# Kernel tuning notes

Hardware: AMD Instinct MI355X
Metric: run time of the kernel (lower is better)

Reference implementation:

```python
import jax, jax.numpy as jnp
import numpy as np

B, T = 4, 2048
IN_H, OUT_H = 4096, 4096   # in_hidden_size = output features, out_hidden_size = input features (torch F.linear quirk)
RANK = 1024


def setup_inputs() -> dict:
    key = jax.random.key(0)
    kx, ku, ks, kv, kb = jax.random.split(key, 5)
    x = jax.random.normal(kx, (B, T, OUT_H), dtype=jnp.float32)
    U = jax.random.normal(ku, (IN_H, RANK), dtype=jnp.float32) * 0.02
    S = jax.random.uniform(ks, (RANK,), dtype=jnp.float32)
    V = jax.random.normal(kv, (OUT_H, RANK), dtype=jnp.float32) * 0.02
    bias = jax.random.normal(kb, (IN_H,), dtype=jnp.float32) * 0.01
    return {"x": x, "U": U, "S": S, "V": V, "bias": bias}


def reference(x, U, S, V, bias):
    # Faithful to torch: M = U @ diag(S) @ V.T  (shape [in_hidden, out_hidden]);
    # F.linear(x, M, bias) = x @ M.T + bias, so x:[...,out_hidden] -> out:[...,in_hidden]
    M = (U * S) @ V.T                     # [IN_H, OUT_H]; (U*S) == U @ diag(S)
    return jnp.einsum('bto,io->bti', x, M) + bias
```

## Files before the change

### kernel.cpp

```cpp
#include <hip/hip_runtime.h>
#include <stdint.h>

typedef __attribute__((ext_vector_type(4))) float  floatx4;
typedef __attribute__((ext_vector_type(8))) short  short8;
typedef __attribute__((ext_vector_type(8))) __bf16 bf16x8;

__device__ __forceinline__ unsigned short f2bf(float f) {
  unsigned int u = __builtin_bit_cast(unsigned int, f);
  u += 0x7fffu + ((u >> 16) & 1u);
  return (unsigned short)(u >> 16);
}

typedef const __attribute__((address_space(1))) void* gptr_t;
typedef __attribute__((address_space(3))) void*       lptr_t;

__global__ __launch_bounds__(256) void prep_fused(
    const float* __restrict__ X, const float* __restrict__ V,
    const float* __restrict__ U, const float* __restrict__ S,
    unsigned short* __restrict__ Xb, unsigned short* __restrict__ Vt,
    unsigned short* __restrict__ Ub,
    int castBlocks, int transTotal, int transGX, int vrows, int vcols,
    unsigned int rankMask) {
  __shared__ float tile[32][33];
  int bid = blockIdx.x;
  int tid = threadIdx.x;
  if (bid < castBlocks) {
    size_t i = ((size_t)bid * 256 + tid) * 8;
    const floatx4* p = (const floatx4*)(X + i);
    floatx4 a = p[0], b = p[1];
    union { unsigned short us[8]; short8 v; } o;
    o.us[0] = f2bf(a[0]); o.us[1] = f2bf(a[1]); o.us[2] = f2bf(a[2]); o.us[3] = f2bf(a[3]);
    o.us[4] = f2bf(b[0]); o.us[5] = f2bf(b[1]); o.us[6] = f2bf(b[2]); o.us[7] = f2bf(b[3]);
    *(short8*)(Xb + i) = o.v;
  } else if (bid < castBlocks + transTotal) {
    int b  = bid - castBlocks;
    int bx = (b % transGX) * 32;
    int by = (b / transGX) * 32;
    int tx = tid & 31;
    int ty = tid >> 5;
    for (int i = ty; i < 32; i += 8)
      tile[i][tx] = V[(size_t)(by + i) * vcols + bx + tx];
    __syncthreads();
    for (int i = ty; i < 32; i += 8)
      Vt[(size_t)(bx + i) * vrows + by + tx] = f2bf(tile[tx][i]);
  } else {
    int b = bid - castBlocks - transTotal;
    size_t i = ((size_t)b * 256 + tid) * 4;
    floatx4 u = *(const floatx4*)(U + i);
    floatx4 s = *(const floatx4*)(S + (i & (size_t)rankMask));
    union { unsigned short us[4]; unsigned long long v; } o;
    o.us[0] = f2bf(u[0] * s[0]); o.us[1] = f2bf(u[1] * s[1]);
    o.us[2] = f2bf(u[2] * s[2]); o.us[3] = f2bf(u[3] * s[3]);
    *(unsigned long long*)(Ub + i) = o.v;
  }
}

__global__ __launch_bounds__(256, 2)
void gemm1_kernel(const unsigned short* __restrict__ A,
                  const unsigned short* __restrict__ Bt,
                  unsigned short* __restrict__ C,
                  int N, int K, int GX) {
  __shared__ unsigned short sA[2][128 * 32];
  __shared__ unsigned short sB[2][128 * 32];

  const int tid  = threadIdx.x;
  const int lane = tid & 63;
  const int wave = tid >> 6;
  const int wm = (wave >> 1) * 64;
  const int wn = (wave & 1) * 64;

  unsigned bid  = blockIdx.x;
  unsigned bw   = 8u * GX;
  unsigned band = bid / bw, rem = bid % bw;
  unsigned by   = band * 8 + (rem & 7u);
  unsigned bx   = rem >> 3;
  const int row0 = by * 128, col0 = bx * 128;

  floatx4 acc[4][4];
#pragma unroll
  for (int i = 0; i < 4; ++i)
#pragma unroll
    for (int j = 0; j < 4; ++j) acc[i][j] = (floatx4){0.f, 0.f, 0.f, 0.f};

  const unsigned short* Ablk = A + (size_t)row0 * K;
  const unsigned short* Bblk = Bt + (size_t)col0 * K;

  const int r0 = tid >> 2, c0 = (tid & 3) * 8;
  const int ldso0 = (wave * 64) * 8;
  const int ldso1 = (256 + wave * 64) * 8;
  const int mrow = lane & 15, quad = lane >> 4;

  for (int k0 = 0; k0 < K; k0 += 64) {
#pragma unroll
    for (int t = 0; t < 2; ++t) {
      const int kk = k0 + t * 32;
      __builtin_amdgcn_global_load_lds((gptr_t)(Ablk + (size_t)r0 * K + kk + c0),
                                       (lptr_t)(sA[t] + ldso0), 16, 0, 0);
      __builtin_amdgcn_global_load_lds((gptr_t)(Ablk + (size_t)(r0 + 64) * K + kk + c0),
                                       (lptr_t)(sA[t] + ldso1), 16, 0, 0);
      __builtin_amdgcn_global_load_lds((gptr_t)(Bblk + (size_t)r0 * K + kk + c0),
                                       (lptr_t)(sB[t] + ldso0), 16, 0, 0);
      __builtin_amdgcn_global_load_lds((gptr_t)(Bblk + (size_t)(r0 + 64) * K + kk + c0),
                                       (lptr_t)(sB[t] + ldso1), 16, 0, 0);
    }
    __syncthreads();
#pragma unroll
    for (int t = 0; t < 2; ++t) {
      bf16x8 af[4], bfr[4];
#pragma unroll
      for (int mi = 0; mi < 4; ++mi)
        af[mi] = __builtin_bit_cast(bf16x8,
                  *(const short8*)(sA[t] + (wm + mi * 16 + mrow) * 32 + quad * 8));
#pragma unroll
      for (int ni = 0; ni < 4; ++ni)
        bfr[ni] = __builtin_bit_cast(bf16x8,
                  *(const short8*)(sB[t] + (wn + ni * 16 + mrow) * 32 + quad * 8));
#pragma unroll
      for (int mi = 0; mi < 4; ++mi)
#pragma unroll
        for (int ni = 0; ni < 4; ++ni)
          acc[mi][ni] = __builtin_amdgcn_mfma_f32_16x16x32_bf16(af[mi], bfr[ni],
                                                                acc[mi][ni], 0, 0, 0);
    }
    __syncthreads();
  }

  const int orow = row0 + wm + quad * 4;
  const int ocol = col0 + wn + mrow;
#pragma unroll
  for (int mi = 0; mi < 4; ++mi)
#pragma unroll
    for (int r = 0; r < 4; ++r) {
      size_t rowoff = (size_t)(orow + mi * 16 + r) * N;
#pragma unroll
      for (int ni = 0; ni < 4; ++ni)
        C[rowoff + ocol + ni * 16] = f2bf(acc[mi][ni][r]);
    }
}

__global__ __launch_bounds__(256, 2)
void gemm2_kernel(const unsigned short* __restrict__ A,
                  const unsigned short* __restrict__ Bt,
                  float* __restrict__ C, const float* __restrict__ bias,
                  int N, int K, int GX) {
  __shared__ unsigned short sA[256 * 32];
  __shared__ unsigned short sB[128 * 32];

  const int tid  = threadIdx.x;
  const int lane = tid & 63;
  const int wave = tid >> 6;
  const int wm = (wave >> 1) * 128;
  const int wn = (wave & 1) * 64;

  unsigned bid  = blockIdx.x;
  unsigned bw   = 8u * GX;
  unsigned band = bid / bw, rem = bid % bw;
  unsigned by   = band * 8 + (rem & 7u);
  unsigned bx   = rem >> 3;
  const int row0 = by * 256, col0 = bx * 128;

  floatx4 acc[8][4];
#pragma unroll
  for (int i = 0; i < 8; ++i)
#pragma unroll
    for (int j = 0; j < 4; ++j) acc[i][j] = (floatx4){0.f, 0.f, 0.f, 0.f};

  const unsigned short* Ablk = A + (size_t)row0 * K;
  const unsigned short* Bblk = Bt + (size_t)col0 * K;

  const int r0 = tid >> 2, c0 = (tid & 3) * 8;
  const int mrow = lane & 15, quad = lane >> 4;

  for (int k0 = 0; k0 < K; k0 += 32) {
#pragma unroll
    for (int j = 0; j < 4; ++j)
      __builtin_amdgcn_global_load_lds((gptr_t)(Ablk + (size_t)(r0 + j * 64) * K + k0 + c0),
                                       (lptr_t)(sA + (j * 256 + wave * 64) * 8), 16, 0, 0);
#pragma unroll
    for (int j = 0; j < 2; ++j)
      __builtin_amdgcn_global_load_lds((gptr_t)(Bblk + (size_t)(r0 + j * 64) * K + k0 + c0),
                                       (lptr_t)(sB + (j * 256 + wave * 64) * 8), 16, 0, 0);
    __syncthreads();

    bf16x8 af[8], bfr[4];
#pragma unroll
    for (int mi = 0; mi < 8; ++mi)
      af[mi] = __builtin_bit_cast(bf16x8,
                *(const short8*)(sA + (wm + mi * 16 + mrow) * 32 + quad * 8));
#pragma unroll
    for (int ni = 0; ni < 4; ++ni)
      bfr[ni] = __builtin_bit_cast(bf16x8,
                *(const short8*)(sB + (wn + ni * 16 + mrow) * 32 + quad * 8));
#pragma unroll
    for (int mi = 0; mi < 8; ++mi)
#pragma unroll
      for (int ni = 0; ni < 4; ++ni)
        acc[mi][ni] = __builtin_amdgcn_mfma_f32_16x16x32_bf16(af[mi], bfr[ni],
                                                              acc[mi][ni], 0, 0, 0);
    __syncthreads();
  }

  const int orow = row0 + wm + quad * 4;
  const int ocol = col0 + wn + mrow;
  float bv[4];
#pragma unroll
  for (int ni = 0; ni < 4; ++ni) bv[ni] = bias[ocol + ni * 16];
#pragma unroll
  for (int mi = 0; mi < 8; ++mi)
#pragma unroll
    for (int r = 0; r < 4; ++r) {
      size_t rowoff = (size_t)(orow + mi * 16 + r) * N;
#pragma unroll
      for (int ni = 0; ni < 4; ++ni)
        C[rowoff + ocol + ni * 16] = acc[mi][ni][r] + bv[ni];
    }
}

extern "C" void kernel_launch(void* const* d_in, const int* in_sizes, int n_in,
                              void* d_out, int out_size, void* d_ws, size_t ws_size,
                              hipStream_t stream) {
  const float* x    = (const float*)d_in[0];
  const float* U    = (const float*)d_in[1];
  const float* S    = (const float*)d_in[2];
  const float* V    = (const float*)d_in[3];
  const float* bias = (const float*)d_in[4];

  const int RANK = in_sizes[2];
  const int INH  = in_sizes[4];
  const int OUTH = in_sizes[3] / RANK;
  const int M    = in_sizes[0] / OUTH;

  unsigned short* Xb = (unsigned short*)d_ws;
  unsigned short* Vt = Xb + (size_t)M * OUTH;
  unsigned short* Ub = Vt + (size_t)RANK * OUTH;
  unsigned short* Yb = Ub + (size_t)INH * RANK;

  const int castBlocks = (int)(((size_t)M * OUTH) / 2048);
  const int transGX    = RANK / 32;
  const int transTotal = transGX * (OUTH / 32);
  const int prepUBlk   = (int)(((size_t)INH * RANK) / 1024);
  prep_fused<<<castBlocks + transTotal + prepUBlk, 256, 0, stream>>>(
      x, V, U, S, Xb, Vt, Ub, castBlocks, transTotal, transGX, OUTH, RANK,
      (unsigned)(RANK - 1));

  gemm1_kernel<<<(M / 128) * (RANK / 128), 256, 0, stream>>>(
      Xb, Vt, Yb, RANK, OUTH, RANK / 128);

  gemm2_kernel<<<(M / 256) * (INH / 128), 256, 0, stream>>>(
      Yb, Ub, (float*)d_out, bias, INH, RANK, INH / 128);
}
```

Baseline: 407.0 us.

## Restructure gemm2 with 256x256 tiles, 512 threads, double-buffered K=64 swizzled LDS

The second GEMM moves from a 256x128 tile with 4 waves to a 256x256 tile with 8 waves. It also uses a BK=64, double-buffered LDS pipeline with an XOR swizzle, prefetches two stages ahead, and raises wave priority around the MFMA bursts. The aim is to hide global-to-LDS load latency behind compute, cut LDS bank conflicts, and improve operand reuse per block. In exchange it uses 128 KB of LDS per block, which limits occupancy, and it adds more complex wait-count synchronization.

Result: faster. 397.8 us (-2.3%).

```diff
diff --git a/kernel.cpp b/kernel.cpp
--- a/kernel.cpp
+++ b/kernel.cpp
@@ -138,26 +138,26 @@
     }
 }
 
-__global__ __launch_bounds__(256, 2)
+__global__ __launch_bounds__(512, 2)
 void gemm2_kernel(const unsigned short* __restrict__ A,
                   const unsigned short* __restrict__ Bt,
                   float* __restrict__ C, const float* __restrict__ bias,
                   int N, int K, int GX) {
-  __shared__ unsigned short sA[256 * 32];
-  __shared__ unsigned short sB[128 * 32];
+  __shared__ unsigned short sA[2][256 * 64];
+  __shared__ unsigned short sB[2][256 * 64];
 
   const int tid  = threadIdx.x;
   const int lane = tid & 63;
   const int wave = tid >> 6;
-  const int wm = (wave >> 1) * 128;
-  const int wn = (wave & 1) * 64;
+  const int wm = (wave >> 2) * 128;
+  const int wn = (wave & 3) * 64;
 
   unsigned bid  = blockIdx.x;
   unsigned bw   = 8u * GX;
   unsigned band = bid / bw, rem = bid % bw;
   unsigned by   = band * 8 + (rem & 7u);
   unsigned bx   = rem >> 3;
-  const int row0 = by * 256, col0 = bx * 128;
+  const int row0 = by * 256, col0 = bx * 256;
 
   floatx4 acc[8][4];
 #pragma unroll
@@ -165,40 +165,80 @@
 #pragma unroll
     for (int j = 0; j < 4; ++j) acc[i][j] = (floatx4){0.f, 0.f, 0.f, 0.f};
 
-  const unsigned short* Ablk = A + (size_t)row0 * K;
-  const unsigned short* Bblk = Bt + (size_t)col0 * K;
-
-  const int r0 = tid >> 2, c0 = (tid & 3) * 8;
+  const int srow = wave * 8 + (lane >> 3);
+  const int ssl  = (lane & 7) ^ (lane >> 3);
+  const unsigned short* Ag = A  + (size_t)(row0 + srow) * K + ssl * 8;
+  const unsigned short* Bg = Bt + (size_t)(col0 + srow) * K + ssl * 8;
+  const int ldsw = (wave * 8) * 64;
+
   const int mrow = lane & 15, quad = lane >> 4;
-
-  for (int k0 = 0; k0 < K; k0 += 32) {
-#pragma unroll
-    for (int j = 0; j < 4; ++j)
-      __builtin_amdgcn_global_load_lds((gptr_t)(Ablk + (size_t)(r0 + j * 64) * K + k0 + c0),
-                                       (lptr_t)(sA + (j * 256 + wave * 64) * 8), 16, 0, 0);
-#pragma unroll
-    for (int j = 0; j < 2; ++j)
-      __builtin_amdgcn_global_load_lds((gptr_t)(Bblk + (size_t)(r0 + j * 64) * K + k0 + c0),
-                                       (lptr_t)(sB + (j * 256 + wave * 64) * 8), 16, 0, 0);
-    __syncthreads();
-
-    bf16x8 af[8], bfr[4];
-#pragma unroll
-    for (int mi = 0; mi < 8; ++mi)
-      af[mi] = __builtin_bit_cast(bf16x8,
-                *(const short8*)(sA + (wm + mi * 16 + mrow) * 32 + quad * 8));
-#pragma unroll
-    for (int ni = 0; ni < 4; ++ni)
-      bfr[ni] = __builtin_bit_cast(bf16x8,
-                *(const short8*)(sB + (wn + ni * 16 + mrow) * 32 + quad * 8));
-#pragma unroll
-    for (int mi = 0; mi < 8; ++mi)
-#pragma unroll
-      for (int ni = 0; ni < 4; ++ni)
-        acc[mi][ni] = __builtin_amdgcn_mfma_f32_16x16x32_bf16(af[mi], bfr[ni],
-                                                              acc[mi][ni], 0, 0, 0);
-    __syncthreads();
-  }
+  const int sw = mrow & 7;
+  const int paof[2] = { (wm + mrow) * 64 + ((quad ^ sw) << 3),
+                        (wm + mrow) * 64 + (((quad + 4) ^ sw) << 3) };
+  const int pbof[2] = { (wn + mrow) * 64 + ((quad ^ sw) << 3),
+                        (wn + mrow) * 64 + (((quad + 4) ^ sw) << 3) };
+
+  const int NKT = K >> 6;
+
+#define STAGE_G2(KOFF, BUF)                                                    \
+  {                                                                            \
+    const unsigned short* As_ = Ag + (KOFF);                                   \
+    const unsigned short* Bs_ = Bg + (KOFF);                                   \
+    unsigned short* dA_ = &sA[(BUF)][0] + ldsw;                                \
+    unsigned short* dB_ = &sB[(BUF)][0] + ldsw;                                \
+    _Pragma("unroll")                                                          \
+    for (int j_ = 0; j_ < 4; ++j_) {                                           \
+      __builtin_amdgcn_global_load_lds((gptr_t)(As_ + (size_t)j_ * 64 * K),    \
+                                       (lptr_t)(dA_ + j_ * 4096), 16, 0, 0);   \
+      __builtin_amdgcn_global_load_lds((gptr_t)(Bs_ + (size_t)j_ * 64 * K),    \
+                                       (lptr_t)(dB_ + j_ * 4096), 16, 0, 0);   \
+    }                                                                          \
+  }
+
+  STAGE_G2(0, 0);
+  STAGE_G2(64, 1);
+  asm volatile("s_waitcnt vmcnt(8)" ::: "memory");
+  __builtin_amdgcn_s_barrier();
+
+  int cur = 0;
+  for (int kt = 0; kt < NKT; ++kt) {
+    const unsigned short* bA = &sA[cur][0];
+    const unsigned short* bB = &sB[cur][0];
+#pragma unroll
+    for (int ks = 0; ks < 2; ++ks) {
+      bf16x8 bfr[4], af[8];
+#pragma unroll
+      for (int ni = 0; ni < 4; ++ni)
+        bfr[ni] = __builtin_bit_cast(bf16x8,
+                    *(const short8*)(bB + pbof[ks] + ni * 1024));
+#pragma unroll
+      for (int mi = 0; mi < 8; ++mi)
+        af[mi] = __builtin_bit_cast(bf16x8,
+                    *(const short8*)(bA + paof[ks] + mi * 1024));
+      __builtin_amdgcn_s_setprio(1);
+#pragma unroll
+      for (int mi = 0; mi < 8; ++mi)
+#pragma unroll
+        for (int ni = 0; ni < 4; ++ni)
+          acc[mi][ni] = __builtin_amdgcn_mfma_f32_16x16x32_bf16(af[mi], bfr[ni],
+                                                                acc[mi][ni], 0, 0, 0);
+      __builtin_amdgcn_s_setprio(0);
+    }
+    asm volatile("s_waitcnt lgkmcnt(0)" ::: "memory");
+    __builtin_amdgcn_sched_barrier(0);
+    __builtin_amdgcn_s_barrier();
+    __builtin_amdgcn_sched_barrier(0);
+    if (kt + 2 < NKT) {
+      STAGE_G2((kt + 2) * 64, cur);
+      asm volatile("s_waitcnt vmcnt(8)" ::: "memory");
+      __builtin_amdgcn_s_barrier();
+    } else if (kt + 1 < NKT) {
+      asm volatile("s_waitcnt vmcnt(0)" ::: "memory");
+      __builtin_amdgcn_s_barrier();
+    }
+    cur ^= 1;
+  }
+#undef STAGE_G2
 
   const int orow = row0 + wm + quad * 4;
   const int ocol = col0 + wn + mrow;
@@ -246,6 +286,6 @@
   gemm1_kernel<<<(M / 128) * (RANK / 128), 256, 0, stream>>>(
       Xb, Vt, Yb, RANK, OUTH, RANK / 128);
 
-  gemm2_kernel<<<(M / 256) * (INH / 128), 256, 0, stream>>>(
-      Yb, Ub, (float*)d_out, bias, INH, RANK, INH / 128);
-}
+  gemm2_kernel<<<(M / 256) * (INH / 256), 512, 0, stream>>>(
+      Yb, Ub, (float*)d_out, bias, INH, RANK, INH / 256);
+}
```
